# Kernel optimization log

Measured on AMD Instinct MI355X. Metric: run time of the kernel, lower is better.

## Reference

```python
import jax, jax.numpy as jnp
import numpy as np

N_NODES = 100000
N_EDGES = 3200000


def _gcn_conv(x, src, dst, W, b, n_nodes):
    # PyG GCNConv: out = D^{-1/2} (A + I) D^{-1/2} X W + b
    h = x @ W  # [N, out]
    # degree of (A + I) counted at targets (symmetric graph assumption as in PyG norm)
    deg = jax.ops.segment_sum(jnp.ones_like(dst, dtype=h.dtype), dst, num_segments=n_nodes)
    dinv = jnp.where(deg > 0, jax.lax.rsqrt(deg), 0.0)
    norm = dinv[src] * dinv[dst]  # [E_total]
    msg = h[src] * norm[:, None]  # gather + normalize  [E_total, out]
    out = jax.ops.segment_sum(msg, dst, num_segments=n_nodes)  # scatter-add
    return out + b


def setup_inputs() -> dict:
    key = jax.random.key(0)
    k1, k2, k3, k4 = jax.random.split(key, 4)
    x = jax.random.normal(k1, (N_NODES, 1), dtype=jnp.float32)
    edge_index = jax.random.randint(k2, (2, N_EDGES), 0, N_NODES, dtype=jnp.int64)
    W1 = jax.random.normal(k3, (1, 64), dtype=jnp.float32) * (1.0 / np.sqrt(1.0))
    b1 = jnp.zeros((64,), dtype=jnp.float32)
    W2 = jax.random.normal(k4, (64, 2), dtype=jnp.float32) * (1.0 / np.sqrt(64.0))
    b2 = jnp.zeros((2,), dtype=jnp.float32)
    return {"x": x, "edge_index": edge_index, "W1": W1, "b1": b1, "W2": W2, "b2": b2}


def reference(x, edge_index, W1, b1, W2, b2):
    n = x.shape[0]
    # add self-loops as GCNConv does by default
    loops = jnp.arange(n, dtype=edge_index.dtype)
    src = jnp.concatenate([edge_index[0], loops])
    dst = jnp.concatenate([edge_index[1], loops])
    h = _gcn_conv(x, src, dst, W1, b1, n)
    h = jax.nn.relu(h)
    h = _gcn_conv(h, src, dst, W2, b2, n)
    h = jax.nn.log_softmax(h, axis=1)
    out = jnp.mean(h, axis=0)
    return out[None, :]  # [1, 2]
```

## Files before the change

### kernel.cpp

```cpp
#include <hip/hip_runtime.h>


#define TPB 512
#define SORT_BLK 256
#define BSHIFT 7
#define BNODES 128
#define MAXBUCK 1024
#define BSTRIDE 6144


__global__ __launch_bounds__(TPB) void k_sort(const int* __restrict__ ei, int E, int epb,
                                              int nbuck, int* __restrict__ gcur,
                                              unsigned* __restrict__ packed) {
    __shared__ int h[MAXBUCK];
    for (int b = threadIdx.x; b < nbuck; b += TPB) h[b] = 0;
    __syncthreads();
    const int4* d4 = (const int4*)(ei + E);
    int nq = epb >> 2;
    int q0 = blockIdx.x * nq;
    for (int j = threadIdx.x; j < nq; j += TPB) {
        int q = q0 + j;
        int e = q << 2;
        if (e + 3 < E) {
            int4 v = d4[q];
            atomicAdd(&h[v.x >> BSHIFT], 1);
            atomicAdd(&h[v.y >> BSHIFT], 1);
            atomicAdd(&h[v.z >> BSHIFT], 1);
            atomicAdd(&h[v.w >> BSHIFT], 1);
        } else {
            for (int k = 0; k < 4; ++k)
                if (e + k < E) atomicAdd(&h[(ei + E)[e + k] >> BSHIFT], 1);
        }
    }
    __syncthreads();
    for (int b = threadIdx.x; b < nbuck; b += TPB) {
        int c = h[b];
        h[b] = c ? atomicAdd(&gcur[b], c) : 0;
    }
    __syncthreads();
    const int4* s4 = (const int4*)ei;
    for (int j = threadIdx.x; j < nq; j += TPB) {
        int q = q0 + j;
        int e = q << 2;
        if (e + 3 < E) {
            int4 vs = s4[q];
            int4 vd = d4[q];
            int b, p;
            b = vd.x >> BSHIFT; p = atomicAdd(&h[b], 1);
            packed[b * BSTRIDE + p] = ((unsigned)(vd.x & (BNODES - 1)) << 17) | (unsigned)vs.x;
            b = vd.y >> BSHIFT; p = atomicAdd(&h[b], 1);
            packed[b * BSTRIDE + p] = ((unsigned)(vd.y & (BNODES - 1)) << 17) | (unsigned)vs.y;
            b = vd.z >> BSHIFT; p = atomicAdd(&h[b], 1);
            packed[b * BSTRIDE + p] = ((unsigned)(vd.z & (BNODES - 1)) << 17) | (unsigned)vs.z;
            b = vd.w >> BSHIFT; p = atomicAdd(&h[b], 1);
            packed[b * BSTRIDE + p] = ((unsigned)(vd.w & (BNODES - 1)) << 17) | (unsigned)vs.w;
        } else {
            for (int k = 0; k < 4; ++k) {
                int ee = e + k;
                if (ee < E) {
                    int s = ei[ee], d = ei[E + ee];
                    int b = d >> BSHIFT;
                    int p = atomicAdd(&h[b], 1);
                    packed[b * BSTRIDE + p] = ((unsigned)(d & (BNODES - 1)) << 17) | (unsigned)s;
                }
            }
        }
    }
}


__global__ __launch_bounds__(TPB) void k_csr(unsigned* __restrict__ packed,
                                             const int* __restrict__ gcur,
                                             const float* __restrict__ x,
                                             float* __restrict__ dinv,
                                             float* __restrict__ u,
                                             int* __restrict__ rptr, int N) {
    __shared__ int cnt[8][BNODES];
    __shared__ int eptr[BNODES];
    __shared__ unsigned stage[BSTRIDE];
    const int tid = threadIdx.x;
    for (int k = tid; k < 8 * BNODES; k += TPB) ((int*)cnt)[k] = 0;
    __syncthreads();
    int b = blockIdx.x;
    int sz = gcur[b];
    unsigned* base = packed + (size_t)b * BSTRIDE;
    const uint4* base4 = (const uint4*)base;
    int wv = tid >> 6;
    int nq4 = sz >> 2;
    int half = nq4 >> 1;
    for (int j = tid; j < half; j += TPB) {
        uint4 p = base4[j];
        uint4 q = base4[j + half];
        atomicAdd(&cnt[wv][(p.x >> 17) & 127], 1);
        atomicAdd(&cnt[wv][(p.y >> 17) & 127], 1);
        atomicAdd(&cnt[wv][(p.z >> 17) & 127], 1);
        atomicAdd(&cnt[wv][(p.w >> 17) & 127], 1);
        atomicAdd(&cnt[wv][(q.x >> 17) & 127], 1);
        atomicAdd(&cnt[wv][(q.y >> 17) & 127], 1);
        atomicAdd(&cnt[wv][(q.z >> 17) & 127], 1);
        atomicAdd(&cnt[wv][(q.w >> 17) & 127], 1);
    }
    for (int j = half * 8 + tid; j < sz; j += TPB) {
        unsigned p = base[j];
        atomicAdd(&cnt[wv][(p >> 17) & 127], 1);
    }
    __syncthreads();
    int tot = 0;
    if (tid < BNODES) {
        #pragma unroll
        for (int c = 0; c < 8; ++c) tot += cnt[c][tid];
        eptr[tid] = tot;
    }
    __syncthreads();
    if (tid < 64) {
        int v0 = eptr[tid], v1 = eptr[tid + 64];
        #pragma unroll
        for (int off = 1; off < 64; off <<= 1) {
            int t0 = __shfl_up(v0, off, 64);
            int t1 = __shfl_up(v1, off, 64);
            if (tid >= off) { v0 += t0; v1 += t1; }
        }
        v1 += __shfl(v0, 63, 64);
        eptr[tid] = v0;
        eptr[tid + 64] = v1;
    }
    __syncthreads();
    if (tid < BNODES) {
        int t = tid;
        int ex = eptr[t] - tot;
        int run = ex;
        #pragma unroll
        for (int c = 0; c < 8; ++c) { int v = cnt[c][t]; cnt[c][t] = run; run += v; }
        rptr[b * BNODES + t] = ex;
        int node = (b << BSHIFT) + t;
        if (node < N) {
            float di = rsqrtf((float)(tot + 1));
            dinv[node] = di;
            u[node] = di * x[node];
        }
    }
    __syncthreads();
    for (int j = tid; j < half; j += TPB) {
        uint4 p = base4[j];
        uint4 q = base4[j + half];
        int pos;
        pos = atomicAdd(&cnt[wv][(p.x >> 17) & 127], 1); stage[pos] = p.x & 0x1FFFF;
        pos = atomicAdd(&cnt[wv][(p.y >> 17) & 127], 1); stage[pos] = p.y & 0x1FFFF;
        pos = atomicAdd(&cnt[wv][(p.z >> 17) & 127], 1); stage[pos] = p.z & 0x1FFFF;
        pos = atomicAdd(&cnt[wv][(p.w >> 17) & 127], 1); stage[pos] = p.w & 0x1FFFF;
        pos = atomicAdd(&cnt[wv][(q.x >> 17) & 127], 1); stage[pos] = q.x & 0x1FFFF;
        pos = atomicAdd(&cnt[wv][(q.y >> 17) & 127], 1); stage[pos] = q.y & 0x1FFFF;
        pos = atomicAdd(&cnt[wv][(q.z >> 17) & 127], 1); stage[pos] = q.z & 0x1FFFF;
        pos = atomicAdd(&cnt[wv][(q.w >> 17) & 127], 1); stage[pos] = q.w & 0x1FFFF;
    }
    for (int j = half * 8 + tid; j < sz; j += TPB) {
        unsigned p = base[j];
        int pos = atomicAdd(&cnt[wv][(p >> 17) & 127], 1);
        stage[pos] = p & 0x1FFFF;
    }
    __syncthreads();
    for (int k = tid; k < sz; k += TPB) base[k] = stage[k];
}


__global__ __launch_bounds__(TPB) void k_agg1(const unsigned* __restrict__ sorted,
                                              const int* __restrict__ gcur,
                                              const int* __restrict__ rptr,
                                              const float* __restrict__ dinv,
                                              const float* __restrict__ u,
                                              const float* __restrict__ W1,
                                              const float* __restrict__ b1,
                                              const float* __restrict__ W2,
                                              float2* __restrict__ w, int N) {
    __shared__ float sW1[64], sb1[64], sW2[128];
    __shared__ int sptr[BNODES + 1];
    int b = blockIdx.x;
    if (threadIdx.x < 64) { sW1[threadIdx.x] = W1[threadIdx.x]; sb1[threadIdx.x] = b1[threadIdx.x]; }
    else if (threadIdx.x < 192) sW2[threadIdx.x - 64] = W2[threadIdx.x - 64];
    if (threadIdx.x < BNODES) sptr[threadIdx.x] = rptr[b * BNODES + threadIdx.x];
    if (threadIdx.x == 0) sptr[BNODES] = gcur[b];
    __syncthreads();
    int t = threadIdx.x >> 2, k = threadIdx.x & 3;
    const unsigned* base = sorted + (size_t)b * BSTRIDE;
    int s0 = sptr[t], s1 = sptr[t + 1];
    float s = 0.f;
    int j = s0 + k;
    for (; j + 12 < s1; j += 16) {
        unsigned i0 = base[j], i1 = base[j + 4], i2 = base[j + 8], i3 = base[j + 12];
        float a0 = u[i0], a1 = u[i1], a2 = u[i2], a3 = u[i3];
        s += (a0 + a1) + (a2 + a3);
    }
    for (; j < s1; j += 4) s += u[base[j]];
    s += __shfl_xor(s, 1, 64);
    s += __shfl_xor(s, 2, 64);
    int node = (b << BSHIFT) + t;
    if (k == 0 && node < N) {
        float di = dinv[node];
        float sv = di * (s + u[node]);
        float z0 = 0.f, z1 = 0.f;
        #pragma unroll
        for (int jj = 0; jj < 64; ++jj) {
            float h = fmaxf(fmaf(sv, sW1[jj], sb1[jj]), 0.f);
            z0 = fmaf(h, sW2[2 * jj], z0);
            z1 = fmaf(h, sW2[2 * jj + 1], z1);
        }
        w[node] = make_float2(di * z0, di * z1);
    }
}


__global__ __launch_bounds__(TPB) void k_agg2(const unsigned* __restrict__ sorted,
                                              const int* __restrict__ gcur,
                                              const int* __restrict__ rptr,
                                              const float* __restrict__ dinv,
                                              const float2* __restrict__ w,
                                              const float* __restrict__ b2,
                                              float* __restrict__ accum, int N) {
    __shared__ int sptr[BNODES + 1];
    int b = blockIdx.x;
    if (threadIdx.x < BNODES) sptr[threadIdx.x] = rptr[b * BNODES + threadIdx.x];
    if (threadIdx.x == 0) sptr[BNODES] = gcur[b];
    __syncthreads();
    int t = threadIdx.x >> 2, k = threadIdx.x & 3;
    const unsigned* base = sorted + (size_t)b * BSTRIDE;
    int s0 = sptr[t], s1 = sptr[t + 1];
    float sx = 0.f, sy = 0.f;
    int j = s0 + k;
    for (; j + 12 < s1; j += 16) {
        unsigned i0 = base[j], i1 = base[j + 4], i2 = base[j + 8], i3 = base[j + 12];
        float2 v0 = w[i0], v1 = w[i1], v2 = w[i2], v3 = w[i3];
        sx += (v0.x + v1.x) + (v2.x + v3.x);
        sy += (v0.y + v1.y) + (v2.y + v3.y);
    }
    for (; j < s1; j += 4) {
        float2 v = w[base[j]];
        sx += v.x;
        sy += v.y;
    }
    sx += __shfl_xor(sx, 1, 64); sx += __shfl_xor(sx, 2, 64);
    sy += __shfl_xor(sy, 1, 64); sy += __shfl_xor(sy, 2, 64);
    int node = (b << BSHIFT) + t;
    float l0 = 0.f, l1 = 0.f;
    if (k == 0 && node < N) {
        float di = dinv[node];
        float2 wi = w[node];
        float a0 = di * (sx + wi.x) + b2[0];
        float a1 = di * (sy + wi.y) + b2[1];
        float m = fmaxf(a0, a1);
        float lse = m + logf(expf(a0 - m) + expf(a1 - m));
        l0 = a0 - lse;
        l1 = a1 - lse;
    }
    #pragma unroll
    for (int off = 32; off > 0; off >>= 1) {
        l0 += __shfl_down(l0, off, 64);
        l1 += __shfl_down(l1, off, 64);
    }
    __shared__ float r0[TPB / 64], r1[TPB / 64];
    int wid = threadIdx.x >> 6, lane = threadIdx.x & 63;
    if (lane == 0) { r0[wid] = l0; r1[wid] = l1; }
    __syncthreads();
    if (threadIdx.x == 0) {
        float t0 = 0.f, t1 = 0.f;
        #pragma unroll
        for (int kk = 0; kk < TPB / 64; ++kk) { t0 += r0[kk]; t1 += r1[kk]; }
        accum[2 * b]     = t0;
        accum[2 * b + 1] = t1;
    }
}


#define RTPB 1024
__global__ __launch_bounds__(RTPB) void k_reduce_final(const float* __restrict__ accum,
                                                       int nb, float* __restrict__ out,
                                                       float invN) {
    float t0 = 0.f, t1 = 0.f;
    for (int i = threadIdx.x; i < nb; i += RTPB) {
        t0 += accum[2 * i];
        t1 += accum[2 * i + 1];
    }
    #pragma unroll
    for (int off = 32; off > 0; off >>= 1) {
        t0 += __shfl_down(t0, off, 64);
        t1 += __shfl_down(t1, off, 64);
    }
    __shared__ float s0[RTPB / 64], s1[RTPB / 64];
    int wid = threadIdx.x >> 6, lane = threadIdx.x & 63;
    if (lane == 0) { s0[wid] = t0; s1[wid] = t1; }
    __syncthreads();
    if (threadIdx.x == 0) {
        float a = 0.f, b = 0.f;
        #pragma unroll
        for (int k = 0; k < RTPB / 64; ++k) { a += s0[k]; b += s1[k]; }
        out[0] = a * invN;
        out[1] = b * invN;
    }
}

__global__ void k_finalize(const float* __restrict__ accum, float* __restrict__ out, float invN) {
    out[0] = accum[0] * invN;
    out[1] = accum[1] * invN;
}


#define FTPB 256
__global__ void k_hist(const int* __restrict__ dst, int E, int* __restrict__ deg) {
    int e = blockIdx.x * FTPB + threadIdx.x;
    if (e < E) atomicAdd(&deg[dst[e]], 1);
}
__global__ void k_dinv_u(const int* __restrict__ deg, const float* __restrict__ x,
                         float* __restrict__ dinv, float* __restrict__ u, int N) {
    int i = blockIdx.x * FTPB + threadIdx.x;
    if (i < N) {
        float di = rsqrtf((float)(deg[i] + 1));
        dinv[i] = di;
        u[i] = di * x[i];
    }
}
__global__ void k_scatter1(const int* __restrict__ ei, int E,
                           const float* __restrict__ u, float* __restrict__ t) {
    int e = blockIdx.x * FTPB + threadIdx.x;
    if (e < E) atomicAdd(&t[ei[E + e]], u[ei[e]]);
}
__global__ void k_node_mid_fb(const float* __restrict__ dinv, const float* __restrict__ u,
                              const float* __restrict__ t,
                              const float* __restrict__ W1, const float* __restrict__ b1,
                              const float* __restrict__ W2, float2* __restrict__ w, int N) {
    __shared__ float sW1[64], sb1[64], sW2[128];
    if (threadIdx.x < 64) { sW1[threadIdx.x] = W1[threadIdx.x]; sb1[threadIdx.x] = b1[threadIdx.x]; }
    if (threadIdx.x < 128) sW2[threadIdx.x] = W2[threadIdx.x];
    __syncthreads();
    int i = blockIdx.x * FTPB + threadIdx.x;
    if (i < N) {
        float di = dinv[i];
        float s = di * (t[i] + u[i]);
        float z0 = 0.f, z1 = 0.f;
        #pragma unroll
        for (int j = 0; j < 64; ++j) {
            float h = fmaxf(fmaf(s, sW1[j], sb1[j]), 0.f);
            z0 = fmaf(h, sW2[2 * j], z0);
            z1 = fmaf(h, sW2[2 * j + 1], z1);
        }
        w[i] = make_float2(di * z0, di * z1);
    }
}
__global__ void k_scatter2(const int* __restrict__ ei, int E,
                           const float2* __restrict__ w, float* __restrict__ acc) {
    int e = blockIdx.x * FTPB + threadIdx.x;
    if (e < E) {
        float2 ws = w[ei[e]];
        int d = ei[E + e];
        atomicAdd(&acc[2 * d], ws.x);
        atomicAdd(&acc[2 * d + 1], ws.y);
    }
}
__global__ void k_node_out_fb(const float* __restrict__ dinv, const float2* __restrict__ w,
                              const float2* __restrict__ acc, const float* __restrict__ b2,
                              float* __restrict__ accum, int N) {
    int i = blockIdx.x * FTPB + threadIdx.x;
    float l0 = 0.f, l1 = 0.f;
    if (i < N) {
        float di = dinv[i];
        float2 a = acc[i];
        float2 ww = w[i];
        float a0 = di * (a.x + ww.x) + b2[0];
        float a1 = di * (a.y + ww.y) + b2[1];
        float m = fmaxf(a0, a1);
        float lse = m + logf(expf(a0 - m) + expf(a1 - m));
        l0 = a0 - lse;
        l1 = a1 - lse;
    }
    #pragma unroll
    for (int off = 32; off > 0; off >>= 1) {
        l0 += __shfl_down(l0, off, 64);
        l1 += __shfl_down(l1, off, 64);
    }
    __shared__ float s0[FTPB / 64], s1[FTPB / 64];
    int wid = threadIdx.x >> 6, lane = threadIdx.x & 63;
    if (lane == 0) { s0[wid] = l0; s1[wid] = l1; }
    __syncthreads();
    if (threadIdx.x == 0) {
        float t0 = 0.f, t1 = 0.f;
        #pragma unroll
        for (int k = 0; k < FTPB / 64; ++k) { t0 += s0[k]; t1 += s1[k]; }
        atomicAdd(&accum[0], t0);
        atomicAdd(&accum[1], t1);
    }
}

extern "C" void kernel_launch(void* const* d_in, const int* in_sizes, int n_in,
                              void* d_out, int out_size, void* d_ws, size_t ws_size,
                              hipStream_t stream) {
    const float* x  = (const float*)d_in[0];
    const int*   ei = (const int*)d_in[1];
    const float* W1 = (const float*)d_in[2];
    const float* b1 = (const float*)d_in[3];
    const float* W2 = (const float*)d_in[4];
    const float* b2 = (const float*)d_in[5];
    float* out = (float*)d_out;

    const int N = in_sizes[0];
    const int E = in_sizes[1] / 2;
    const int nbuck = (N + BNODES - 1) >> BSHIFT;
    const int gridN = (N + FTPB - 1) / FTPB;
    const int gridE = (E + FTPB - 1) / FTPB;

    size_t offPacked = 0;
    size_t offW      = offPacked + (size_t)nbuck * BSTRIDE * 4;
    size_t offDinv   = offW + (size_t)N * 8;
    size_t offU      = offDinv + (size_t)N * 4;
    size_t offGcur   = offU + (size_t)N * 4;
    size_t offAccum  = offGcur + (size_t)nbuck * 4;
    size_t offRptr   = offAccum + (size_t)2 * nbuck * 4;
    size_t need      = offRptr + (size_t)nbuck * BNODES * 4;

    if (ws_size >= need && nbuck <= MAXBUCK && N <= (1 << 17)) {
        unsigned* packed = (unsigned*)((char*)d_ws + offPacked);
        float2*   w      = (float2*)((char*)d_ws + offW);
        float*    dinv   = (float*)((char*)d_ws + offDinv);
        float*    u      = (float*)((char*)d_ws + offU);
        int*      gcur   = (int*)((char*)d_ws + offGcur);
        float*    accum  = (float*)((char*)d_ws + offAccum);
        int*      rptr   = (int*)((char*)d_ws + offRptr);

        hipMemsetAsync(gcur, 0, (size_t)nbuck * 4, stream);

        int epb = (((E + SORT_BLK - 1) / SORT_BLK) + 3) & ~3;

        k_sort<<<SORT_BLK, TPB, 0, stream>>>(ei, E, epb, nbuck, gcur, packed);
        k_csr<<<nbuck, TPB, 0, stream>>>(packed, gcur, x, dinv, u, rptr, N);
        k_agg1<<<nbuck, TPB, 0, stream>>>(packed, gcur, rptr, dinv, u, W1, b1, W2, w, N);
        k_agg2<<<nbuck, TPB, 0, stream>>>(packed, gcur, rptr, dinv, (const float2*)w, b2, accum, N);
        k_reduce_final<<<1, RTPB, 0, stream>>>(accum, nbuck, out, 1.0f / (float)N);
    } else {
        int*   deg   = (int*)d_ws;
        float* t     = (float*)(deg + N);
        float* acc   = t + N;
        float* accum = acc + 2 * N;
        float* dinv  = accum + 2;
        float* u     = dinv + N;
        float2* w    = (float2*)(u + N);
        hipMemsetAsync(d_ws, 0, (size_t)(4 * N + 2) * sizeof(float), stream);
        k_hist<<<gridE, FTPB, 0, stream>>>(ei + E, E, deg);
        k_dinv_u<<<gridN, FTPB, 0, stream>>>(deg, x, dinv, u, N);
        k_scatter1<<<gridE, FTPB, 0, stream>>>(ei, E, u, t);
        k_node_mid_fb<<<gridN, FTPB, 0, stream>>>(dinv, u, t, W1, b1, W2, w, N);
        k_scatter2<<<gridE, FTPB, 0, stream>>>(ei, E, w, acc);
        k_node_out_fb<<<gridN, FTPB, 0, stream>>>(dinv, w, (const float2*)acc, b2, accum, N);
        k_finalize<<<1, 64, 0, stream>>>(accum, out, 1.0f / (float)N);
    }
}
```

Before: 159.4 us.

## Move CSR placement into layer-1 aggregation kernel, aggregating from shared staging

Splits the CSR-building kernel into a count-only kernel and a kernel that performs the per-bucket placement into shared memory and immediately aggregates layer 1 from that staged buffer. This avoids agg1 re-reading the sorted indices from global memory. The placement atomics now use one shared counter per node rather than per-wave counters, which may increase LDS atomic contention. The larger shared footprint in the aggregation kernel could reduce occupancy.

```diff
diff --git a/kernel.cpp b/kernel.cpp
--- a/kernel.cpp
+++ b/kernel.cpp
@@ -69,41 +69,32 @@
 }
 
 
-__global__ __launch_bounds__(TPB) void k_csr(unsigned* __restrict__ packed,
-                                             const int* __restrict__ gcur,
-                                             const float* __restrict__ x,
-                                             float* __restrict__ dinv,
-                                             float* __restrict__ u,
-                                             int* __restrict__ rptr, int N) {
+__global__ __launch_bounds__(TPB) void k_count(const unsigned* __restrict__ packed,
+                                               const int* __restrict__ gcur,
+                                               const float* __restrict__ x,
+                                               float* __restrict__ dinv,
+                                               float* __restrict__ u,
+                                               int* __restrict__ rptr, int N) {
     __shared__ int cnt[8][BNODES];
     __shared__ int eptr[BNODES];
-    __shared__ unsigned stage[BSTRIDE];
     const int tid = threadIdx.x;
     for (int k = tid; k < 8 * BNODES; k += TPB) ((int*)cnt)[k] = 0;
     __syncthreads();
-    int b = blockIdx.x;
-    int sz = gcur[b];
-    unsigned* base = packed + (size_t)b * BSTRIDE;
+    const int b = blockIdx.x;
+    const int sz = gcur[b];
+    const unsigned* base = packed + (size_t)b * BSTRIDE;
     const uint4* base4 = (const uint4*)base;
-    int wv = tid >> 6;
-    int nq4 = sz >> 2;
-    int half = nq4 >> 1;
-    for (int j = tid; j < half; j += TPB) {
+    const int wv = tid >> 6;
+    const int nq4 = sz >> 2;
+    for (int j = tid; j < nq4; j += TPB) {
         uint4 p = base4[j];
-        uint4 q = base4[j + half];
         atomicAdd(&cnt[wv][(p.x >> 17) & 127], 1);
         atomicAdd(&cnt[wv][(p.y >> 17) & 127], 1);
         atomicAdd(&cnt[wv][(p.z >> 17) & 127], 1);
         atomicAdd(&cnt[wv][(p.w >> 17) & 127], 1);
-        atomicAdd(&cnt[wv][(q.x >> 17) & 127], 1);
-        atomicAdd(&cnt[wv][(q.y >> 17) & 127], 1);
-        atomicAdd(&cnt[wv][(q.z >> 17) & 127], 1);
-        atomicAdd(&cnt[wv][(q.w >> 17) & 127], 1);
-    }
-    for (int j = half * 8 + tid; j < sz; j += TPB) {
-        unsigned p = base[j];
-        atomicAdd(&cnt[wv][(p >> 17) & 127], 1);
-    }
+    }
+    for (int j = (nq4 << 2) + tid; j < sz; j += TPB)
+        atomicAdd(&cnt[wv][(base[j] >> 17) & 127], 1);
     __syncthreads();
     int tot = 0;
     if (tid < BNODES) {
@@ -126,71 +117,70 @@
     }
     __syncthreads();
     if (tid < BNODES) {
-        int t = tid;
-        int ex = eptr[t] - tot;
-        int run = ex;
-        #pragma unroll
-        for (int c = 0; c < 8; ++c) { int v = cnt[c][t]; cnt[c][t] = run; run += v; }
-        rptr[b * BNODES + t] = ex;
-        int node = (b << BSHIFT) + t;
+        int ex = eptr[tid] - tot;
+        rptr[b * BNODES + tid] = ex;
+        int node = (b << BSHIFT) + tid;
         if (node < N) {
             float di = rsqrtf((float)(tot + 1));
             dinv[node] = di;
             u[node] = di * x[node];
         }
     }
-    __syncthreads();
-    for (int j = tid; j < half; j += TPB) {
+}
+
+
+__global__ __launch_bounds__(TPB) void k_place_agg1(unsigned* __restrict__ packed,
+                                                    const int* __restrict__ gcur,
+                                                    const int* __restrict__ rptr,
+                                                    const float* __restrict__ dinv,
+                                                    const float* __restrict__ u,
+                                                    const float* __restrict__ W1,
+                                                    const float* __restrict__ b1,
+                                                    const float* __restrict__ W2,
+                                                    float2* __restrict__ w, int N) {
+    __shared__ unsigned stage[BSTRIDE];
+    __shared__ int sptr[BNODES + 1];
+    __shared__ int cur[BNODES];
+    __shared__ float sW1[64], sb1[64], sW2[128];
+    const int tid = threadIdx.x;
+    const int b = blockIdx.x;
+    if (tid < 64) { sW1[tid] = W1[tid]; sb1[tid] = b1[tid]; }
+    else if (tid < 192) sW2[tid - 64] = W2[tid - 64];
+    if (tid < BNODES) {
+        int v = rptr[b * BNODES + tid];
+        sptr[tid] = v;
+        cur[tid] = v;
+    }
+    if (tid == 0) sptr[BNODES] = gcur[b];
+    __syncthreads();
+    const int sz = sptr[BNODES];
+    unsigned* base = packed + (size_t)b * BSTRIDE;
+    const uint4* base4 = (const uint4*)base;
+    const int nq4 = sz >> 2;
+    for (int j = tid; j < nq4; j += TPB) {
         uint4 p = base4[j];
-        uint4 q = base4[j + half];
         int pos;
-        pos = atomicAdd(&cnt[wv][(p.x >> 17) & 127], 1); stage[pos] = p.x & 0x1FFFF;
-        pos = atomicAdd(&cnt[wv][(p.y >> 17) & 127], 1); stage[pos] = p.y & 0x1FFFF;
-        pos = atomicAdd(&cnt[wv][(p.z >> 17) & 127], 1); stage[pos] = p.z & 0x1FFFF;
-        pos = atomicAdd(&cnt[wv][(p.w >> 17) & 127], 1); stage[pos] = p.w & 0x1FFFF;
-        pos = atomicAdd(&cnt[wv][(q.x >> 17) & 127], 1); stage[pos] = q.x & 0x1FFFF;
-        pos = atomicAdd(&cnt[wv][(q.y >> 17) & 127], 1); stage[pos] = q.y & 0x1FFFF;
-        pos = atomicAdd(&cnt[wv][(q.z >> 17) & 127], 1); stage[pos] = q.z & 0x1FFFF;
-        pos = atomicAdd(&cnt[wv][(q.w >> 17) & 127], 1); stage[pos] = q.w & 0x1FFFF;
-    }
-    for (int j = half * 8 + tid; j < sz; j += TPB) {
+        pos = atomicAdd(&cur[(p.x >> 17) & 127], 1); stage[pos] = p.x & 0x1FFFF;
+        pos = atomicAdd(&cur[(p.y >> 17) & 127], 1); stage[pos] = p.y & 0x1FFFF;
+        pos = atomicAdd(&cur[(p.z >> 17) & 127], 1); stage[pos] = p.z & 0x1FFFF;
+        pos = atomicAdd(&cur[(p.w >> 17) & 127], 1); stage[pos] = p.w & 0x1FFFF;
+    }
+    for (int j = (nq4 << 2) + tid; j < sz; j += TPB) {
         unsigned p = base[j];
-        int pos = atomicAdd(&cnt[wv][(p >> 17) & 127], 1);
+        int pos = atomicAdd(&cur[(p >> 17) & 127], 1);
         stage[pos] = p & 0x1FFFF;
     }
     __syncthreads();
-    for (int k = tid; k < sz; k += TPB) base[k] = stage[k];
-}
-
-
-__global__ __launch_bounds__(TPB) void k_agg1(const unsigned* __restrict__ sorted,
-                                              const int* __restrict__ gcur,
-                                              const int* __restrict__ rptr,
-                                              const float* __restrict__ dinv,
-                                              const float* __restrict__ u,
-                                              const float* __restrict__ W1,
-                                              const float* __restrict__ b1,
-                                              const float* __restrict__ W2,
-                                              float2* __restrict__ w, int N) {
-    __shared__ float sW1[64], sb1[64], sW2[128];
-    __shared__ int sptr[BNODES + 1];
-    int b = blockIdx.x;
-    if (threadIdx.x < 64) { sW1[threadIdx.x] = W1[threadIdx.x]; sb1[threadIdx.x] = b1[threadIdx.x]; }
-    else if (threadIdx.x < 192) sW2[threadIdx.x - 64] = W2[threadIdx.x - 64];
-    if (threadIdx.x < BNODES) sptr[threadIdx.x] = rptr[b * BNODES + threadIdx.x];
-    if (threadIdx.x == 0) sptr[BNODES] = gcur[b];
-    __syncthreads();
-    int t = threadIdx.x >> 2, k = threadIdx.x & 3;
-    const unsigned* base = sorted + (size_t)b * BSTRIDE;
+    int t = tid >> 2, k = tid & 3;
     int s0 = sptr[t], s1 = sptr[t + 1];
     float s = 0.f;
     int j = s0 + k;
     for (; j + 12 < s1; j += 16) {
-        unsigned i0 = base[j], i1 = base[j + 4], i2 = base[j + 8], i3 = base[j + 12];
+        unsigned i0 = stage[j], i1 = stage[j + 4], i2 = stage[j + 8], i3 = stage[j + 12];
         float a0 = u[i0], a1 = u[i1], a2 = u[i2], a3 = u[i3];
         s += (a0 + a1) + (a2 + a3);
     }
-    for (; j < s1; j += 4) s += u[base[j]];
+    for (; j < s1; j += 4) s += u[stage[j]];
     s += __shfl_xor(s, 1, 64);
     s += __shfl_xor(s, 2, 64);
     int node = (b << BSHIFT) + t;
@@ -206,6 +196,7 @@
         }
         w[node] = make_float2(di * z0, di * z1);
     }
+    for (int k2 = tid; k2 < sz; k2 += TPB) base[k2] = stage[k2];
 }
 
 
@@ -428,8 +419,8 @@
         int epb = (((E + SORT_BLK - 1) / SORT_BLK) + 3) & ~3;
 
         k_sort<<<SORT_BLK, TPB, 0, stream>>>(ei, E, epb, nbuck, gcur, packed);
-        k_csr<<<nbuck, TPB, 0, stream>>>(packed, gcur, x, dinv, u, rptr, N);
-        k_agg1<<<nbuck, TPB, 0, stream>>>(packed, gcur, rptr, dinv, u, W1, b1, W2, w, N);
+        k_count<<<nbuck, TPB, 0, stream>>>(packed, gcur, x, dinv, u, rptr, N);
+        k_place_agg1<<<nbuck, TPB, 0, stream>>>(packed, gcur, rptr, dinv, u, W1, b1, W2, w, N);
         k_agg2<<<nbuck, TPB, 0, stream>>>(packed, gcur, rptr, dinv, (const float2*)w, b2, accum, N);
         k_reduce_final<<<1, RTPB, 0, stream>>>(accum, nbuck, out, 1.0f / (float)N);
     } else {
```

Result: no change. 157.3 us (-1.3%).
